# Optimization experiments

Hardware: AMD Instinct MI355X
Metric: run time of the kernel (lower is better)

Reference implementation:

```python
import jax, jax.numpy as jnp
import numpy as np

B, S, D = 32, 2048, 64
DK, DV = 24, 32

def setup_inputs() -> dict:
    key = jax.random.key(0)
    ks = jax.random.split(key, 5)
    # PyTorch nn.Linear(in,out) weight is [out,in]; we store transposed [in,out]
    # so y = x @ W matches x @ weight.T. Kaiming-uniform-ish scale.
    def init(k, fan_in, shape):
        bound = 1.0 / np.sqrt(fan_in)
        return jax.random.uniform(k, shape, jnp.float32, -bound, bound)
    return {
        "x": jax.random.normal(ks[0], (B, S, D), jnp.float32),
        "Wq": init(ks[1], D, (D, DK)),
        "Wk": init(ks[2], D, (D, DK)),
        "Wv": init(ks[3], D, (D, DV)),
        "Wh": init(ks[4], DV, (DV, D)),
    }

def reference(x, Wq, Wk, Wv, Wh):
    # x: [B,S,64]
    q = jnp.einsum("bsd,dk->bsk", x, Wq)          # [B,S,24]
    k = jnp.einsum("bsd,dk->bsk", x, Wk)          # [B,S,24]
    v = jnp.einsum("bsd,dk->bsk", x, Wv)          # [B,S,32]
    a = jnp.einsum("bqk,btk->bqt", q, k)          # [B,S,S], q @ k^T
    # NOTE: softmax over dim=1 (the query axis), as in the original module.
    a = jax.nn.softmax(a, axis=1)
    h1 = jnp.einsum("bqt,btv->bqv", a, v)         # [B,S,32]
    return jnp.einsum("bqv,vd->bqd", h1, Wh)      # [B,S,64]
```

## Files before the change

### kernel.cpp

```cpp
#include <hip/hip_runtime.h>
#include <hip/hip_bf16.h>

#define NB 32
#define NS 2048
#define ND 64
#define NDK 24
#define NDV 32
#define LOG2E 1.4426950408889634f

typedef __attribute__((ext_vector_type(8))) short short8;
typedef __attribute__((ext_vector_type(4))) float f32x4;

typedef __attribute__((address_space(3))) unsigned int lds_u32;
typedef __attribute__((address_space(1))) const unsigned int glb_u32;

__device__ __forceinline__ void cp16(const void* g, void* l) {
  __builtin_amdgcn_global_load_lds((glb_u32*)g, (lds_u32*)l, 16, 0, 0);
}

__device__ __forceinline__ float fexp2(float x) {
  return __builtin_amdgcn_exp2f(x);
}

__device__ __forceinline__ unsigned pk2(float a, float b) {
  __hip_bfloat16 ha = __float2bfloat16(a), hb = __float2bfloat16(b);
  return ((unsigned)__builtin_bit_cast(unsigned short, hb) << 16) |
         (unsigned)__builtin_bit_cast(unsigned short, ha);
}

__device__ __forceinline__ unsigned pku(__hip_bfloat16 lo, __hip_bfloat16 hi) {
  return ((unsigned)__builtin_bit_cast(unsigned short, hi) << 16) |
         (unsigned)__builtin_bit_cast(unsigned short, lo);
}


__global__ __launch_bounds__(256) void prep_kernel(
    const float* __restrict__ Wq, const float* __restrict__ Wk,
    const float* __restrict__ Wv, const float* __restrict__ Wh,
    __hip_bfloat16* __restrict__ wt, __hip_bfloat16* __restrict__ whT) {
  const int tid = threadIdx.x;
  for (int o = tid; o < 6144; o += 256) {
    const int n = o / 72, d = o % 72;
    float val = 0.f;
    if (o < 5760 && d < ND) {
      if (n < 24)      val = Wq[d * NDK + n] * LOG2E;
      else if (n < 48) val = Wk[d * NDK + (n - 24)];
      else             val = Wv[d * NDV + (n - 48)];
    }
    wt[o] = __float2bfloat16(val);
  }
  {
    const int lane = tid & 63, l15 = lane & 15, lg = lane >> 4;
    const int d = (tid >> 6) * 16 + l15;
    uint4 u;
    u.x = pk2(Wh[(lg * 8 + 0) * ND + d], Wh[(lg * 8 + 1) * ND + d]);
    u.y = pk2(Wh[(lg * 8 + 2) * ND + d], Wh[(lg * 8 + 3) * ND + d]);
    u.z = pk2(Wh[(lg * 8 + 4) * ND + d], Wh[(lg * 8 + 5) * ND + d]);
    u.w = pk2(Wh[(lg * 8 + 6) * ND + d], Wh[(lg * 8 + 7) * ND + d]);
    ((uint4*)whT)[tid] = u;
  }
}

__global__ __launch_bounds__(256) void proj_kernel(
    const float* __restrict__ x, const __hip_bfloat16* __restrict__ wt,
    __hip_bfloat16* __restrict__ qfb, __hip_bfloat16* __restrict__ kfb,
    __hip_bfloat16* __restrict__ vfb) {
  __shared__ __hip_bfloat16 xsb[64 * 72];
  __shared__ __hip_bfloat16 Wt[6144];
  __shared__ __hip_bfloat16 os[64][81];

  const int tid = threadIdx.x;
  const size_t row0 = (size_t)blockIdx.x * 64;
  const int b = (int)(row0 >> 11);
  const int tile = (int)((row0 >> 6) & 31);
  const int wv = tid >> 6, lane = tid & 63;
  const int l15 = lane & 15, lg = lane >> 4;

  #pragma unroll
  for (int i = 0; i < 3; ++i)
    cp16((const char*)wt + (i * 256 + tid) * 16, (char*)Wt + (i * 256 + tid) * 16);

  {
    const int r = tid >> 2, c16 = (tid & 3) * 16;
    const float4* src = (const float4*)(x + (row0 + r) * ND + c16);
    unsigned u[8];
    #pragma unroll
    for (int i = 0; i < 4; ++i) {
      float4 f = src[i];
      u[2 * i] = pk2(f.x, f.y);
      u[2 * i + 1] = pk2(f.z, f.w);
    }
    uint4* dst = (uint4*)((char*)xsb + r * 144 + c16 * 2);
    dst[0] = make_uint4(u[0], u[1], u[2], u[3]);
    dst[1] = make_uint4(u[4], u[5], u[6], u[7]);
  }
  __syncthreads();

  {
    short8 a[2];
    #pragma unroll
    for (int kc = 0; kc < 2; ++kc)
      a[kc] = *(const short8*)((char*)xsb + ((wv * 16 + l15) * 72 + kc * 32 + lg * 8) * 2);
    const f32x4 z = {0.f, 0.f, 0.f, 0.f};
    #pragma unroll
    for (int nt = 0; nt < 5; ++nt) {
      f32x4 acc = z;
      #pragma unroll
      for (int kc = 0; kc < 2; ++kc) {
        const short8 bfr = *(const short8*)((char*)Wt + ((nt * 16 + l15) * 72 + kc * 32 + lg * 8) * 2);
        acc = __builtin_amdgcn_mfma_f32_16x16x32_bf16(a[kc], bfr, acc, 0, 0, 0);
      }
      #pragma unroll
      for (int r = 0; r < 4; ++r)
        os[wv * 16 + lg * 4 + r][nt * 16 + l15] = __float2bfloat16(acc[r]);
    }
  }
  __syncthreads();

  const size_t fbase = ((size_t)(b * 32 + tile)) * 4 * 256;
  for (int j = tid; j < 2048; j += 256) {
    const int arr = j >> 10, jj = j & 1023;
    const int qs = jj >> 8, ln = (jj >> 2) & 63, wd = jj & 3;
    const int row = qs * 16 + (ln & 15);
    const int c0 = (ln >> 4) * 8 + wd * 2;
    unsigned u = 0;
    if (c0 < 24) u = pku(os[row][arr * 24 + c0], os[row][arr * 24 + c0 + 1]);
    unsigned* dst = (unsigned*)(arr ? kfb : qfb);
    dst[fbase + (size_t)qs * 256 + ln * 4 + wd] = u;
  }
  for (int j = tid; j < 1024; j += 256) {
    const int fi = j >> 8;
    const int ln = (j >> 2) & 63, wd = j & 3;
    const int v = (fi & 1) * 16 + (ln & 15);
    const int tl = (fi >> 1) * 32 + (ln >> 4) * 8 + wd * 2;
    const unsigned u = pku(os[tl][48 + v], os[tl + 1][48 + v]);
    ((unsigned*)vfb)[fbase + (size_t)fi * 256 + ln * 4 + wd] = u;
  }
}

__global__ __launch_bounds__(256) void stats_kernel(
    const __hip_bfloat16* __restrict__ qfb, const __hip_bfloat16* __restrict__ kfb,
    float* __restrict__ ls) {
  __shared__ __hip_bfloat16 Qs[2][2048];

  const int g = blockIdx.x;
  const int xcd = g & 7, loc = g >> 3;
  const int b = (xcd << 2) + (loc >> 4);
  const int tg = loc & 15;
  const int tid = threadIdx.x;
  const int wv = tid >> 6, lane = tid & 63;
  const int l15 = lane & 15, lg = lane >> 4;
  const int tile_t = tg * 2 + (wv >> 1);
  const int ib = (wv & 1) * 2;

  short8 kf[2];
  #pragma unroll
  for (int j = 0; j < 2; ++j)
    kf[j] = *(const short8*)(kfb + (((size_t)(b * 32 + tile_t)) * 4 + ib + j) * 512 + lane * 8);

  const char* gq = (const char*)(qfb + (size_t)b * 32 * 2048);
  const f32x4 z = {0.f, 0.f, 0.f, 0.f};
  f32x4 s0 = z, s1 = z;

  cp16(gq + tid * 16, (char*)Qs[0] + tid * 16);
  __syncthreads();

  for (int it = 0; it < 32; ++it) {
    const int cur = it & 1;
    if (it + 1 < 32)
      cp16(gq + (size_t)(it + 1) * 4096 + tid * 16, (char*)Qs[cur ^ 1] + tid * 16);
    #pragma unroll
    for (int qi = 0; qi < 4; ++qi) {
      const short8 qfr = *(const short8*)((char*)Qs[cur] + qi * 1024 + lane * 16);
      f32x4 d0 = __builtin_amdgcn_mfma_f32_16x16x32_bf16(kf[0], qfr, z, 0, 0, 0);
      f32x4 d1 = __builtin_amdgcn_mfma_f32_16x16x32_bf16(kf[1], qfr, z, 0, 0, 0);
      #pragma unroll
      for (int r = 0; r < 4; ++r) { s0[r] += fexp2(d0[r]); s1[r] += fexp2(d1[r]); }
    }
    __syncthreads();
  }
  #pragma unroll
  for (int m = 1; m < 16; m <<= 1) {
    #pragma unroll
    for (int r = 0; r < 4; ++r) {
      s0[r] += __shfl_xor(s0[r], m);
      s1[r] += __shfl_xor(s1[r], m);
    }
  }
  if (l15 == 0) {
    f32x4 o0, o1;
    #pragma unroll
    for (int r = 0; r < 4; ++r) { o0[r] = -__log2f(s0[r]); o1[r] = -__log2f(s1[r]); }
    float* lp = ls + ((size_t)b << 11) + tile_t * 64 + ib * 16 + lg * 4;
    *(f32x4*)(lp) = o0;
    *(f32x4*)(lp + 16) = o1;
  }
}

__global__ __launch_bounds__(256) void attn_kernel(
    const __hip_bfloat16* __restrict__ qfb, const __hip_bfloat16* __restrict__ kfb,
    const __hip_bfloat16* __restrict__ vfb, const float* __restrict__ ls,
    const __hip_bfloat16* __restrict__ whT, float* __restrict__ out) {
  __shared__ char Ks[2][4096];
  __shared__ char Vs[2][4096];
  __shared__ float lss[2][64];
  __shared__ char Ps[4 * 2304];

  const int g = blockIdx.x;
  const int xcd = g & 7, loc = g >> 3;
  const int b = (xcd << 2) + (loc >> 4);
  const int qg = loc & 15;
  const int tid = threadIdx.x;
  const int wv = tid >> 6, lane = tid & 63;
  const int l15 = lane & 15, lg = lane >> 4;
  const int tile_q = qg * 2 + (wv >> 1);
  const int ib = (wv & 1) * 2;

  char* Pw = Ps + wv * 2304 + l15 * 144;

  short8 qf[2];
  #pragma unroll
  for (int qi = 0; qi < 2; ++qi)
    qf[qi] = *(const short8*)(qfb + (((size_t)(b * 32 + tile_q)) * 4 + ib + qi) * 512 + lane * 8);

  const char* gk = (const char*)(kfb + (size_t)b * 32 * 2048);
  const char* gv = (const char*)(vfb + (size_t)b * 32 * 2048);
  const char* gl = (const char*)(ls + ((size_t)b << 11));

  const f32x4 z = {0.f, 0.f, 0.f, 0.f};
  f32x4 h1[2][2] = {{z, z}, {z, z}};

  cp16(gk + tid * 16, (char*)Ks[0] + tid * 16);
  cp16(gv + tid * 16, (char*)Vs[0] + tid * 16);
  if (tid < 16) cp16(gl + tid * 16, (char*)lss[0] + tid * 16);
  __syncthreads();

  for (int it = 0; it < 32; ++it) {
    const int cur = it & 1;
    if (it + 1 < 32) {
      cp16(gk + (size_t)(it + 1) * 4096 + tid * 16, (char*)Ks[cur ^ 1] + tid * 16);
      cp16(gv + (size_t)(it + 1) * 4096 + tid * 16, (char*)Vs[cur ^ 1] + tid * 16);
      if (tid < 16) cp16(gl + (size_t)(it + 1) * 256 + tid * 16, (char*)lss[cur ^ 1] + tid * 16);
    }
    short8 kfr[4], vfr[2][2];
    f32x4 lsv[4];
    #pragma unroll
    for (int ts = 0; ts < 4; ++ts) {
      kfr[ts] = *(const short8*)(Ks[cur] + ts * 1024 + lane * 16);
      lsv[ts] = *(const f32x4*)(&lss[cur][ts * 16 + lg * 4]);
    }
    #pragma unroll
    for (int kc = 0; kc < 2; ++kc)
      #pragma unroll
      for (int vs = 0; vs < 2; ++vs)
        vfr[kc][vs] = *(const short8*)(Vs[cur] + (kc * 2 + vs) * 1024 + lane * 16);

    #pragma unroll
    for (int qi = 0; qi < 2; ++qi) {
      #pragma unroll
      for (int ts = 0; ts < 4; ++ts) {
        f32x4 d = __builtin_amdgcn_mfma_f32_16x16x32_bf16(kfr[ts], qf[qi], z, 0, 0, 0);
        uint2 w;
        w.x = pk2(fexp2(d[0] + lsv[ts][0]), fexp2(d[1] + lsv[ts][1]));
        w.y = pk2(fexp2(d[2] + lsv[ts][2]), fexp2(d[3] + lsv[ts][3]));
        *(uint2*)(Pw + ts * 32 + lg * 8) = w;
      }
      const short8 p0 = *(const short8*)(Pw + lg * 16);
      const short8 p1 = *(const short8*)(Pw + 64 + lg * 16);
      h1[qi][0] = __builtin_amdgcn_mfma_f32_16x16x32_bf16(p0, vfr[0][0], h1[qi][0], 0, 0, 0);
      h1[qi][1] = __builtin_amdgcn_mfma_f32_16x16x32_bf16(p0, vfr[0][1], h1[qi][1], 0, 0, 0);
      h1[qi][0] = __builtin_amdgcn_mfma_f32_16x16x32_bf16(p1, vfr[1][0], h1[qi][0], 0, 0, 0);
      h1[qi][1] = __builtin_amdgcn_mfma_f32_16x16x32_bf16(p1, vfr[1][1], h1[qi][1], 0, 0, 0);
    }
    __syncthreads();
  }

  short8 wf[4];
  #pragma unroll
  for (int dt = 0; dt < 4; ++dt)
    wf[dt] = *(const short8*)(whT + dt * 512 + lane * 8);
  #pragma unroll
  for (int qi = 0; qi < 2; ++qi) {
    #pragma unroll
    for (int vs = 0; vs < 2; ++vs)
      #pragma unroll
      for (int r = 0; r < 4; ++r)
        *(unsigned short*)(Ps + wv * 2304 + (lg * 4 + r) * 144 + (vs * 16 + l15) * 2) =
            __builtin_bit_cast(unsigned short, __float2bfloat16(h1[qi][vs][r]));
    const short8 hf = *(const short8*)(Pw + lg * 16);
    float* ob = out + (size_t)(b * NS + tile_q * 64 + (ib + qi) * 16 + lg * 4) * ND + l15;
    #pragma unroll
    for (int dt = 0; dt < 4; ++dt) {
      f32x4 o = __builtin_amdgcn_mfma_f32_16x16x32_bf16(hf, wf[dt], z, 0, 0, 0);
      float* op = ob + dt * 16;
      op[0] = o[0];
      op[ND] = o[1];
      op[2 * ND] = o[2];
      op[3 * ND] = o[3];
    }
  }
}

extern "C" void kernel_launch(void* const* d_in, const int* in_sizes, int n_in,
                              void* d_out, int out_size, void* d_ws, size_t ws_size,
                              hipStream_t stream) {
  const float* x  = (const float*)d_in[0];
  const float* Wq = (const float*)d_in[1];
  const float* Wk = (const float*)d_in[2];
  const float* Wv = (const float*)d_in[3];
  const float* Wh = (const float*)d_in[4];
  float* out = (float*)d_out;

  char* ws = (char*)d_ws;
  __hip_bfloat16* qfb = (__hip_bfloat16*)ws;
  __hip_bfloat16* kfb = (__hip_bfloat16*)(ws + 4194304);
  __hip_bfloat16* vfb = (__hip_bfloat16*)(ws + 8388608);
  float*          lsp = (float*)(ws + 12582912);
  __hip_bfloat16* whT = (__hip_bfloat16*)(ws + 12845056);
  __hip_bfloat16* wt  = (__hip_bfloat16*)(ws + 12849152);

  hipLaunchKernelGGL(prep_kernel, dim3(1), dim3(256), 0, stream,
                     Wq, Wk, Wv, Wh, wt, whT);
  hipLaunchKernelGGL(proj_kernel, dim3(1024), dim3(256), 0, stream,
                     x, wt, qfb, kfb, vfb);
  hipLaunchKernelGGL(stats_kernel, dim3(512), dim3(256), 0, stream,
                     qfb, kfb, lsp);
  hipLaunchKernelGGL(attn_kernel, dim3(512), dim3(256), 0, stream,
                     qfb, kfb, vfb, lsp, whT, out);
}
```

Before: 83.84 us.

## Triple-buffer K/V/Q LDS staging with one barrier per iteration and fold lse into MFMA

Both kernels move from double to triple buffering of the LDS tiles. A manual vmcnt wait plus a single s_barrier per iteration replaces the two __syncthreads, and prefetch now runs two tiles ahead. The attention kernel loads the full log-sum row into LDS once up front and passes it as the MFMA accumulator input, which removes four adds per score fragment. Compiler memory fences are added around the per-wave P scratch reuse. This uses more LDS, and it relies on hand-counted vmcnt values being correct.

```diff
diff --git a/kernel.cpp b/kernel.cpp
--- a/kernel.cpp
+++ b/kernel.cpp
@@ -13,6 +13,11 @@
 
 typedef __attribute__((address_space(3))) unsigned int lds_u32;
 typedef __attribute__((address_space(1))) const unsigned int glb_u32;
+
+#define WAITV(N) asm volatile("s_waitcnt vmcnt(" #N ")" ::: "memory")
+#define SBARRIER do { asm volatile("s_barrier" ::: "memory"); \
+                      __builtin_amdgcn_sched_barrier(0); } while (0)
+#define LFENCE asm volatile("" ::: "memory")
 
 __device__ __forceinline__ void cp16(const void* g, void* l) {
   __builtin_amdgcn_global_load_lds((glb_u32*)g, (lds_u32*)l, 16, 0, 0);
@@ -141,7 +146,7 @@
 __global__ __launch_bounds__(256) void stats_kernel(
     const __hip_bfloat16* __restrict__ qfb, const __hip_bfloat16* __restrict__ kfb,
     float* __restrict__ ls) {
-  __shared__ __hip_bfloat16 Qs[2][2048];
+  __shared__ __hip_bfloat16 Qs[3][2048];
 
   const int g = blockIdx.x;
   const int xcd = g & 7, loc = g >> 3;
@@ -163,12 +168,18 @@
   f32x4 s0 = z, s1 = z;
 
   cp16(gq + tid * 16, (char*)Qs[0] + tid * 16);
-  __syncthreads();
-
+  cp16(gq + 4096 + tid * 16, (char*)Qs[1] + tid * 16);
+  WAITV(0);
+  SBARRIER;
+
+  int cur = 0;
   for (int it = 0; it < 32; ++it) {
-    const int cur = it & 1;
-    if (it + 1 < 32)
-      cp16(gq + (size_t)(it + 1) * 4096 + tid * 16, (char*)Qs[cur ^ 1] + tid * 16);
+    if (it < 31) { WAITV(1); } else { WAITV(0); }
+    SBARRIER;
+    if (it + 2 < 32) {
+      int nx = cur + 2; if (nx >= 3) nx -= 3;
+      cp16(gq + (size_t)(it + 2) * 4096 + tid * 16, (char*)Qs[nx] + tid * 16);
+    }
     #pragma unroll
     for (int qi = 0; qi < 4; ++qi) {
       const short8 qfr = *(const short8*)((char*)Qs[cur] + qi * 1024 + lane * 16);
@@ -177,7 +188,7 @@
       #pragma unroll
       for (int r = 0; r < 4; ++r) { s0[r] += fexp2(d0[r]); s1[r] += fexp2(d1[r]); }
     }
-    __syncthreads();
+    cur = (cur == 2) ? 0 : cur + 1;
   }
   #pragma unroll
   for (int m = 1; m < 16; m <<= 1) {
@@ -201,9 +212,9 @@
     const __hip_bfloat16* __restrict__ qfb, const __hip_bfloat16* __restrict__ kfb,
     const __hip_bfloat16* __restrict__ vfb, const float* __restrict__ ls,
     const __hip_bfloat16* __restrict__ whT, float* __restrict__ out) {
-  __shared__ char Ks[2][4096];
-  __shared__ char Vs[2][4096];
-  __shared__ float lss[2][64];
+  __shared__ char Ks[3][4096];
+  __shared__ char Vs[3][4096];
+  __shared__ float lss[2048];
   __shared__ char Ps[4 * 2304];
 
   const int g = blockIdx.x;
@@ -230,49 +241,55 @@
   const f32x4 z = {0.f, 0.f, 0.f, 0.f};
   f32x4 h1[2][2] = {{z, z}, {z, z}};
 
+  cp16(gl + tid * 16, (char*)lss + tid * 16);
+  cp16(gl + 4096 + tid * 16, (char*)lss + 4096 + tid * 16);
   cp16(gk + tid * 16, (char*)Ks[0] + tid * 16);
   cp16(gv + tid * 16, (char*)Vs[0] + tid * 16);
-  if (tid < 16) cp16(gl + tid * 16, (char*)lss[0] + tid * 16);
-  __syncthreads();
-
+  cp16(gk + 4096 + tid * 16, (char*)Ks[1] + tid * 16);
+  cp16(gv + 4096 + tid * 16, (char*)Vs[1] + tid * 16);
+  WAITV(0);
+  SBARRIER;
+
+  int cur = 0;
   for (int it = 0; it < 32; ++it) {
-    const int cur = it & 1;
-    if (it + 1 < 32) {
-      cp16(gk + (size_t)(it + 1) * 4096 + tid * 16, (char*)Ks[cur ^ 1] + tid * 16);
-      cp16(gv + (size_t)(it + 1) * 4096 + tid * 16, (char*)Vs[cur ^ 1] + tid * 16);
-      if (tid < 16) cp16(gl + (size_t)(it + 1) * 256 + tid * 16, (char*)lss[cur ^ 1] + tid * 16);
-    }
-    short8 kfr[4], vfr[2][2];
+    if (it < 31) { WAITV(2); } else { WAITV(0); }
+    SBARRIER;
+    if (it + 2 < 32) {
+      int nx = cur + 2; if (nx >= 3) nx -= 3;
+      cp16(gk + (size_t)(it + 2) * 4096 + tid * 16, (char*)Ks[nx] + tid * 16);
+      cp16(gv + (size_t)(it + 2) * 4096 + tid * 16, (char*)Vs[nx] + tid * 16);
+    }
+    short8 kfr[4], vfr[4];
     f32x4 lsv[4];
     #pragma unroll
     for (int ts = 0; ts < 4; ++ts) {
       kfr[ts] = *(const short8*)(Ks[cur] + ts * 1024 + lane * 16);
-      lsv[ts] = *(const f32x4*)(&lss[cur][ts * 16 + lg * 4]);
-    }
-    #pragma unroll
-    for (int kc = 0; kc < 2; ++kc)
-      #pragma unroll
-      for (int vs = 0; vs < 2; ++vs)
-        vfr[kc][vs] = *(const short8*)(Vs[cur] + (kc * 2 + vs) * 1024 + lane * 16);
+      lsv[ts] = *(const f32x4*)(lss + it * 64 + ts * 16 + lg * 4);
+    }
+    #pragma unroll
+    for (int f = 0; f < 4; ++f)
+      vfr[f] = *(const short8*)(Vs[cur] + f * 1024 + lane * 16);
 
     #pragma unroll
     for (int qi = 0; qi < 2; ++qi) {
       #pragma unroll
       for (int ts = 0; ts < 4; ++ts) {
-        f32x4 d = __builtin_amdgcn_mfma_f32_16x16x32_bf16(kfr[ts], qf[qi], z, 0, 0, 0);
+        f32x4 d = __builtin_amdgcn_mfma_f32_16x16x32_bf16(kfr[ts], qf[qi], lsv[ts], 0, 0, 0);
         uint2 w;
-        w.x = pk2(fexp2(d[0] + lsv[ts][0]), fexp2(d[1] + lsv[ts][1]));
-        w.y = pk2(fexp2(d[2] + lsv[ts][2]), fexp2(d[3] + lsv[ts][3]));
+        w.x = pk2(fexp2(d[0]), fexp2(d[1]));
+        w.y = pk2(fexp2(d[2]), fexp2(d[3]));
         *(uint2*)(Pw + ts * 32 + lg * 8) = w;
       }
+      LFENCE;
       const short8 p0 = *(const short8*)(Pw + lg * 16);
       const short8 p1 = *(const short8*)(Pw + 64 + lg * 16);
-      h1[qi][0] = __builtin_amdgcn_mfma_f32_16x16x32_bf16(p0, vfr[0][0], h1[qi][0], 0, 0, 0);
-      h1[qi][1] = __builtin_amdgcn_mfma_f32_16x16x32_bf16(p0, vfr[0][1], h1[qi][1], 0, 0, 0);
-      h1[qi][0] = __builtin_amdgcn_mfma_f32_16x16x32_bf16(p1, vfr[1][0], h1[qi][0], 0, 0, 0);
-      h1[qi][1] = __builtin_amdgcn_mfma_f32_16x16x32_bf16(p1, vfr[1][1], h1[qi][1], 0, 0, 0);
-    }
-    __syncthreads();
+      h1[qi][0] = __builtin_amdgcn_mfma_f32_16x16x32_bf16(p0, vfr[0], h1[qi][0], 0, 0, 0);
+      h1[qi][1] = __builtin_amdgcn_mfma_f32_16x16x32_bf16(p0, vfr[1], h1[qi][1], 0, 0, 0);
+      h1[qi][0] = __builtin_amdgcn_mfma_f32_16x16x32_bf16(p1, vfr[2], h1[qi][0], 0, 0, 0);
+      h1[qi][1] = __builtin_amdgcn_mfma_f32_16x16x32_bf16(p1, vfr[3], h1[qi][1], 0, 0, 0);
+      LFENCE;
+    }
+    cur = (cur == 2) ? 0 : cur + 1;
   }
 
   short8 wf[4];
@@ -287,6 +304,7 @@
       for (int r = 0; r < 4; ++r)
         *(unsigned short*)(Ps + wv * 2304 + (lg * 4 + r) * 144 + (vs * 16 + l15) * 2) =
             __builtin_bit_cast(unsigned short, __float2bfloat16(h1[qi][vs][r]));
+    LFENCE;
     const short8 hf = *(const short8*)(Pw + lg * 16);
     float* ob = out + (size_t)(b * NS + tile_q * 64 + (ib + qi) * 16 + lg * 4) * ND + l15;
     #pragma unroll
@@ -298,6 +316,7 @@
       op[2 * ND] = o[2];
       op[3 * ND] = o[3];
     }
+    LFENCE;
   }
 }
 
```

New measurement: 88.57 us. +5.6%, slower.

## Replace LDS-staged K/V/Q tiles with direct register double-buffered global loads

Applied to the files above, without the earlier changes.

Both the stats and attention kernels stop staging K, V, Q and the log-sum tiles through shared memory with global_load_lds and block-wide barriers. Each wave now loads its fragments straight from global memory into register structs, double-buffered across iterations. The log-sum offset is also folded into the MFMA accumulator input instead of being added afterwards. This removes the __syncthreads per iteration and the LDS round trip, but every wave now issues its own redundant global loads (likely L2/L1 hits) and register pressure rises. The P scratch row stride is also changed from 144 to 176 bytes, which alters the LDS bank mapping.

```diff
diff --git a/kernel.cpp b/kernel.cpp
--- a/kernel.cpp
+++ b/kernel.cpp
@@ -13,6 +13,8 @@
 
 typedef __attribute__((address_space(3))) unsigned int lds_u32;
 typedef __attribute__((address_space(1))) const unsigned int glb_u32;
+
+#define LFENCE asm volatile("" ::: "memory")
 
 __device__ __forceinline__ void cp16(const void* g, void* l) {
   __builtin_amdgcn_global_load_lds((glb_u32*)g, (lds_u32*)l, 16, 0, 0);
@@ -138,11 +140,32 @@
   }
 }
 
+struct QT { short8 q0, q1, q2, q3; };
+
+__device__ __forceinline__ void loadQ(QT& t, const __hip_bfloat16* qp, int it, int lane) {
+  const __hip_bfloat16* p = qp + (size_t)it * 2048 + lane * 8;
+  t.q0 = *(const short8*)(p);
+  t.q1 = *(const short8*)(p + 512);
+  t.q2 = *(const short8*)(p + 1024);
+  t.q3 = *(const short8*)(p + 1536);
+}
+
+__device__ __forceinline__ void accQ(const QT& t, short8 kf0, short8 kf1,
+                                     f32x4& s0, f32x4& s1) {
+  const f32x4 z = {0.f, 0.f, 0.f, 0.f};
+  #pragma unroll
+  for (int qi = 0; qi < 4; ++qi) {
+    const short8 q = qi == 0 ? t.q0 : qi == 1 ? t.q1 : qi == 2 ? t.q2 : t.q3;
+    f32x4 d0 = __builtin_amdgcn_mfma_f32_16x16x32_bf16(kf0, q, z, 0, 0, 0);
+    f32x4 d1 = __builtin_amdgcn_mfma_f32_16x16x32_bf16(kf1, q, z, 0, 0, 0);
+    #pragma unroll
+    for (int r = 0; r < 4; ++r) { s0[r] += fexp2(d0[r]); s1[r] += fexp2(d1[r]); }
+  }
+}
+
 __global__ __launch_bounds__(256) void stats_kernel(
     const __hip_bfloat16* __restrict__ qfb, const __hip_bfloat16* __restrict__ kfb,
     float* __restrict__ ls) {
-  __shared__ __hip_bfloat16 Qs[2][2048];
-
   const int g = blockIdx.x;
   const int xcd = g & 7, loc = g >> 3;
   const int b = (xcd << 2) + (loc >> 4);
@@ -158,26 +181,18 @@
   for (int j = 0; j < 2; ++j)
     kf[j] = *(const short8*)(kfb + (((size_t)(b * 32 + tile_t)) * 4 + ib + j) * 512 + lane * 8);
 
-  const char* gq = (const char*)(qfb + (size_t)b * 32 * 2048);
+  const __hip_bfloat16* qp = qfb + (size_t)b * 32 * 2048;
   const f32x4 z = {0.f, 0.f, 0.f, 0.f};
   f32x4 s0 = z, s1 = z;
 
-  cp16(gq + tid * 16, (char*)Qs[0] + tid * 16);
-  __syncthreads();
-
-  for (int it = 0; it < 32; ++it) {
-    const int cur = it & 1;
-    if (it + 1 < 32)
-      cp16(gq + (size_t)(it + 1) * 4096 + tid * 16, (char*)Qs[cur ^ 1] + tid * 16);
-    #pragma unroll
-    for (int qi = 0; qi < 4; ++qi) {
-      const short8 qfr = *(const short8*)((char*)Qs[cur] + qi * 1024 + lane * 16);
-      f32x4 d0 = __builtin_amdgcn_mfma_f32_16x16x32_bf16(kf[0], qfr, z, 0, 0, 0);
-      f32x4 d1 = __builtin_amdgcn_mfma_f32_16x16x32_bf16(kf[1], qfr, z, 0, 0, 0);
-      #pragma unroll
-      for (int r = 0; r < 4; ++r) { s0[r] += fexp2(d0[r]); s1[r] += fexp2(d1[r]); }
-    }
-    __syncthreads();
+  QT A, B;
+  loadQ(A, qp, 0, lane);
+  for (int it2 = 0; it2 < 16; ++it2) {
+    const int itA = it2 * 2;
+    loadQ(B, qp, itA + 1, lane);
+    accQ(A, kf[0], kf[1], s0, s1);
+    loadQ(A, qp, itA + 2 < 32 ? itA + 2 : 31, lane);
+    accQ(B, kf[0], kf[1], s0, s1);
   }
   #pragma unroll
   for (int m = 1; m < 16; m <<= 1) {
@@ -197,14 +212,66 @@
   }
 }
 
+struct KVT {
+  short8 k0, k1, k2, k3;
+  short8 v0, v1, v2, v3;
+  f32x4 l0, l1, l2, l3;
+};
+
+__device__ __forceinline__ void loadKV(KVT& t, const __hip_bfloat16* kp0,
+    const __hip_bfloat16* vp0, const float* lsb, int it, int lane, int lg) {
+  const __hip_bfloat16* kp = kp0 + (size_t)it * 2048 + lane * 8;
+  t.k0 = *(const short8*)(kp);
+  t.k1 = *(const short8*)(kp + 512);
+  t.k2 = *(const short8*)(kp + 1024);
+  t.k3 = *(const short8*)(kp + 1536);
+  const __hip_bfloat16* vp = vp0 + (size_t)it * 2048 + lane * 8;
+  t.v0 = *(const short8*)(vp);
+  t.v1 = *(const short8*)(vp + 512);
+  t.v2 = *(const short8*)(vp + 1024);
+  t.v3 = *(const short8*)(vp + 1536);
+  const float* lp = lsb + it * 64 + lg * 4;
+  t.l0 = *(const f32x4*)(lp);
+  t.l1 = *(const f32x4*)(lp + 16);
+  t.l2 = *(const f32x4*)(lp + 32);
+  t.l3 = *(const f32x4*)(lp + 48);
+}
+
+__device__ __forceinline__ void computeKV(const KVT& t, short8 qf, char* Pw,
+                                          int lg, f32x4& h10, f32x4& h11) {
+  f32x4 d;
+  uint2 w;
+  d = __builtin_amdgcn_mfma_f32_16x16x32_bf16(t.k0, qf, t.l0, 0, 0, 0);
+  w.x = pk2(fexp2(d[0]), fexp2(d[1]));
+  w.y = pk2(fexp2(d[2]), fexp2(d[3]));
+  *(uint2*)(Pw + lg * 8) = w;
+  d = __builtin_amdgcn_mfma_f32_16x16x32_bf16(t.k1, qf, t.l1, 0, 0, 0);
+  w.x = pk2(fexp2(d[0]), fexp2(d[1]));
+  w.y = pk2(fexp2(d[2]), fexp2(d[3]));
+  *(uint2*)(Pw + 32 + lg * 8) = w;
+  d = __builtin_amdgcn_mfma_f32_16x16x32_bf16(t.k2, qf, t.l2, 0, 0, 0);
+  w.x = pk2(fexp2(d[0]), fexp2(d[1]));
+  w.y = pk2(fexp2(d[2]), fexp2(d[3]));
+  *(uint2*)(Pw + 64 + lg * 8) = w;
+  d = __builtin_amdgcn_mfma_f32_16x16x32_bf16(t.k3, qf, t.l3, 0, 0, 0);
+  w.x = pk2(fexp2(d[0]), fexp2(d[1]));
+  w.y = pk2(fexp2(d[2]), fexp2(d[3]));
+  *(uint2*)(Pw + 96 + lg * 8) = w;
+  LFENCE;
+  const short8 p0 = *(const short8*)(Pw + lg * 16);
+  const short8 p1 = *(const short8*)(Pw + 64 + lg * 16);
+  h10 = __builtin_amdgcn_mfma_f32_16x16x32_bf16(p0, t.v0, h10, 0, 0, 0);
+  h11 = __builtin_amdgcn_mfma_f32_16x16x32_bf16(p0, t.v1, h11, 0, 0, 0);
+  h10 = __builtin_amdgcn_mfma_f32_16x16x32_bf16(p1, t.v2, h10, 0, 0, 0);
+  h11 = __builtin_amdgcn_mfma_f32_16x16x32_bf16(p1, t.v3, h11, 0, 0, 0);
+  LFENCE;
+}
+
 __global__ __launch_bounds__(256) void attn_kernel(
     const __hip_bfloat16* __restrict__ qfb, const __hip_bfloat16* __restrict__ kfb,
     const __hip_bfloat16* __restrict__ vfb, const float* __restrict__ ls,
     const __hip_bfloat16* __restrict__ whT, float* __restrict__ out) {
-  __shared__ char Ks[2][4096];
-  __shared__ char Vs[2][4096];
-  __shared__ float lss[2][64];
-  __shared__ char Ps[4 * 2304];
+  __shared__ char Ps[4 * 2816];
 
   const int g = blockIdx.x;
   const int xcd = g & 7, loc = g >> 3;
@@ -216,63 +283,30 @@
   const int tile_q = qg * 2 + (wv >> 1);
   const int ib = (wv & 1) * 2;
 
-  char* Pw = Ps + wv * 2304 + l15 * 144;
+  char* Pw = Ps + wv * 2816 + l15 * 176;
 
   short8 qf[2];
   #pragma unroll
   for (int qi = 0; qi < 2; ++qi)
     qf[qi] = *(const short8*)(qfb + (((size_t)(b * 32 + tile_q)) * 4 + ib + qi) * 512 + lane * 8);
 
-  const char* gk = (const char*)(kfb + (size_t)b * 32 * 2048);
-  const char* gv = (const char*)(vfb + (size_t)b * 32 * 2048);
-  const char* gl = (const char*)(ls + ((size_t)b << 11));
+  const __hip_bfloat16* kp0 = kfb + (size_t)b * 32 * 2048;
+  const __hip_bfloat16* vp0 = vfb + (size_t)b * 32 * 2048;
+  const float* lsb = ls + ((size_t)b << 11);
 
   const f32x4 z = {0.f, 0.f, 0.f, 0.f};
   f32x4 h1[2][2] = {{z, z}, {z, z}};
 
-  cp16(gk + tid * 16, (char*)Ks[0] + tid * 16);
-  cp16(gv + tid * 16, (char*)Vs[0] + tid * 16);
-  if (tid < 16) cp16(gl + tid * 16, (char*)lss[0] + tid * 16);
-  __syncthreads();
-
-  for (int it = 0; it < 32; ++it) {
-    const int cur = it & 1;
-    if (it + 1 < 32) {
-      cp16(gk + (size_t)(it + 1) * 4096 + tid * 16, (char*)Ks[cur ^ 1] + tid * 16);
-      cp16(gv + (size_t)(it + 1) * 4096 + tid * 16, (char*)Vs[cur ^ 1] + tid * 16);
-      if (tid < 16) cp16(gl + (size_t)(it + 1) * 256 + tid * 16, (char*)lss[cur ^ 1] + tid * 16);
-    }
-    short8 kfr[4], vfr[2][2];
-    f32x4 lsv[4];
-    #pragma unroll
-    for (int ts = 0; ts < 4; ++ts) {
-      kfr[ts] = *(const short8*)(Ks[cur] + ts * 1024 + lane * 16);
-      lsv[ts] = *(const f32x4*)(&lss[cur][ts * 16 + lg * 4]);
-    }
-    #pragma unroll
-    for (int kc = 0; kc < 2; ++kc)
-      #pragma unroll
-      for (int vs = 0; vs < 2; ++vs)
-        vfr[kc][vs] = *(const short8*)(Vs[cur] + (kc * 2 + vs) * 1024 + lane * 16);
-
-    #pragma unroll
-    for (int qi = 0; qi < 2; ++qi) {
-      #pragma unroll
-      for (int ts = 0; ts < 4; ++ts) {
-        f32x4 d = __builtin_amdgcn_mfma_f32_16x16x32_bf16(kfr[ts], qf[qi], z, 0, 0, 0);
-        uint2 w;
-        w.x = pk2(fexp2(d[0] + lsv[ts][0]), fexp2(d[1] + lsv[ts][1]));
-        w.y = pk2(fexp2(d[2] + lsv[ts][2]), fexp2(d[3] + lsv[ts][3]));
-        *(uint2*)(Pw + ts * 32 + lg * 8) = w;
-      }
-      const short8 p0 = *(const short8*)(Pw + lg * 16);
-      const short8 p1 = *(const short8*)(Pw + 64 + lg * 16);
-      h1[qi][0] = __builtin_amdgcn_mfma_f32_16x16x32_bf16(p0, vfr[0][0], h1[qi][0], 0, 0, 0);
-      h1[qi][1] = __builtin_amdgcn_mfma_f32_16x16x32_bf16(p0, vfr[0][1], h1[qi][1], 0, 0, 0);
-      h1[qi][0] = __builtin_amdgcn_mfma_f32_16x16x32_bf16(p1, vfr[1][0], h1[qi][0], 0, 0, 0);
-      h1[qi][1] = __builtin_amdgcn_mfma_f32_16x16x32_bf16(p1, vfr[1][1], h1[qi][1], 0, 0, 0);
-    }
-    __syncthreads();
+  KVT A, B;
+  loadKV(A, kp0, vp0, lsb, 0, lane, lg);
+  for (int it2 = 0; it2 < 16; ++it2) {
+    const int itA = it2 * 2;
+    loadKV(B, kp0, vp0, lsb, itA + 1, lane, lg);
+    computeKV(A, qf[0], Pw, lg, h1[0][0], h1[0][1]);
+    computeKV(A, qf[1], Pw, lg, h1[1][0], h1[1][1]);
+    loadKV(A, kp0, vp0, lsb, itA + 2 < 32 ? itA + 2 : 31, lane, lg);
+    computeKV(B, qf[0], Pw, lg, h1[0][0], h1[0][1]);
+    computeKV(B, qf[1], Pw, lg, h1[1][0], h1[1][1]);
   }
 
   short8 wf[4];
@@ -285,8 +319,9 @@
     for (int vs = 0; vs < 2; ++vs)
       #pragma unroll
       for (int r = 0; r < 4; ++r)
-        *(unsigned short*)(Ps + wv * 2304 + (lg * 4 + r) * 144 + (vs * 16 + l15) * 2) =
+        *(unsigned short*)(Ps + wv * 2816 + (lg * 4 + r) * 176 + (vs * 16 + l15) * 2) =
             __builtin_bit_cast(unsigned short, __float2bfloat16(h1[qi][vs][r]));
+    LFENCE;
     const short8 hf = *(const short8*)(Pw + lg * 16);
     float* ob = out + (size_t)(b * NS + tile_q * 64 + (ib + qi) * 16 + lg * 4) * ND + l15;
     #pragma unroll
@@ -298,6 +333,7 @@
       op[2 * ND] = o[2];
       op[3 * ND] = o[3];
     }
+    LFENCE;
   }
 }
 
```

New measurement: 76.65 us. 1.09x faster.
